# Optimization experiments

Hardware: AMD Instinct MI355X
Metric: run time of the kernel (lower is better)

The kernel has to match this reference:

```python
import jax, jax.numpy as jnp
import numpy as np

WS = 8          # window_size
WSU = 2 * WS    # window_size_up
HEADS = 8
SHIFT = WS // 2


def _build_idx(nH, nW):
    # Faithful reproduction of the torch window-reordering index (static numpy).
    if nH % 2 == 0:
        idx_H = np.arange(nH).reshape(2, -1).transpose(1, 0).reshape(-1)
    else:
        idx_H = np.arange(nH + 1).reshape(2, -1).transpose(1, 0).reshape(-1)[:-1]
    if nW % 2 == 0:
        idx_W = np.arange(nW).reshape(2, -1).transpose(1, 0).reshape(-1)
    else:
        idx_W = np.arange(nW + 1).reshape(2, -1).transpose(1, 0).reshape(-1)[:-1]
    idx = np.array([list(idx_W + i * nW) for i in range(nW)])
    return np.asarray(idx[list(idx_H)].reshape(-1))


def _rel_pos_index():
    # coords over the query window offset by ws//2; reference coords over the 2ws x 2ws KV window
    ch = np.arange(WS // 2, WS + WS // 2)
    cw = np.arange(WS // 2, WS + WS // 2)
    coords = np.stack(np.meshgrid(ch, cw, indexing='ij')).reshape(2, -1)        # (2, 64)
    rh = np.arange(2 * WS)
    rw = np.arange(2 * WS)
    ref = np.stack(np.meshgrid(rh, rw, indexing='ij')).reshape(2, -1)           # (2, 256)
    rel = coords[:, :, None] - ref[:, None, :]                                  # (2, 64, 256)
    rel = rel.transpose(1, 2, 0).copy()
    rel[..., 0] += 2 * WS - 1
    rel[..., 1] += 2 * WS - 1
    rel[..., 0] *= 4 * WS - 1
    return rel.sum(-1)  # (64, 256)


def setup_inputs() -> dict:
    key = jax.random.key(0)
    ks = jax.random.split(key, 4)
    C = 256
    return {
        'x': jax.random.normal(ks[0], (8, 128, 128, C), dtype=jnp.float32),
        'mask': jnp.zeros((1, 1, 1), dtype=jnp.float32),  # unused by the module's forward
        'qkv_w': jax.random.normal(ks[1], (3 * C, C), dtype=jnp.float32) * 0.02,
        'qkv_b': jnp.zeros((3 * C,), dtype=jnp.float32),
        'proj_w': jax.random.normal(ks[2], (C, C), dtype=jnp.float32) * 0.02,
        'proj_b': jnp.zeros((C,), dtype=jnp.float32),
        'rel_table': jax.random.normal(ks[3], ((4 * WS - 1) * (4 * WS - 1), HEADS), dtype=jnp.float32) * 0.02,
    }


def reference(x, mask, qkv_w, qkv_b, proj_w, proj_b, rel_table):
    B, H, W, C = x.shape
    hd = C // HEADS
    scale = hd ** (-0.5)

    pad_b = (WS - H % WS) % WS
    pad_r = (WS - W % WS) % WS
    x = jnp.pad(x, ((0, 0), (0, pad_b), (0, pad_r), (0, 0)))
    Hp, Wp = H + pad_b, W + pad_r

    qkv = (x @ qkv_w.T + qkv_b).reshape(B, Hp, Wp, 3, C)
    q = qkv[..., 0, :]                                    # (B, Hp, Wp, C)
    kv = jnp.moveaxis(qkv[..., 1:, :], 3, 0)              # (2, B, Hp, Wp, C)

    # pad KV for cross-window context
    kv = jnp.pad(kv, ((0, 0), (0, 0), (SHIFT, WS - SHIFT), (SHIFT, WS - SHIFT), (0, 0)))
    Hpkv, Wpkv = Hp + WS, Wp + WS

    nH, nW = Hp // WS, Wp // WS
    nHs, nWs = Hpkv // WSU, Wpkv // WSU
    nHsh, nWsh = nH - nHs, nW - nWs

    kv1 = kv[:, :, :nHs * WSU, :nWs * WSU]
    kv2 = kv[:, :, :nHs * WSU, WS:WS + nWsh * WSU]
    kv3 = kv[:, :, WS:WS + nHsh * WSU, :nWs * WSU]
    kv4 = kv[:, :, WS:WS + nHsh * WSU, WS:WS + nWsh * WSU]
    cross = jnp.concatenate([jnp.concatenate([kv1, kv2], axis=3),
                             jnp.concatenate([kv3, kv4], axis=3)], axis=2)

    # window partition at WSU -> (2, B, nH*nW, WSU*WSU, C), then reorder windows
    cross = cross.reshape(2, B, nH, WSU, nW, WSU, C).transpose(0, 1, 2, 4, 3, 5, 6)
    cross = cross.reshape(2, B, nH * nW, WSU * WSU, C)
    cross = cross[:, :, _build_idx(nH, nW)]

    Bw = B * nH * nW
    M = WSU * WSU  # 4*WS*WS KV tokens per window
    N = WS * WS    # query tokens per window
    k = cross[0].reshape(Bw, M, HEADS, hd)
    v = cross[1].reshape(Bw, M, HEADS, hd)

    qw = q.reshape(B, nH, WS, nW, WS, C).transpose(0, 1, 3, 2, 4, 5).reshape(Bw, N, HEADS, hd)

    attn = jnp.einsum('bnhd,bmhd->bhnm', qw * scale, k)   # (Bw, HEADS, N, M)
    bias = rel_table[_rel_pos_index()]                    # (N, M, HEADS)
    attn = jax.nn.softmax(attn + bias.transpose(2, 0, 1)[None], axis=-1)

    out = jnp.einsum('bhnm,bmhd->bnhd', attn, v).reshape(Bw, N, C)
    out = out @ proj_w.T + proj_b

    out = out.reshape(B, nH, nW, WS, WS, C).transpose(0, 1, 3, 2, 4, 5).reshape(B, Hp, Wp, C)
    return out[:, :H, :W, :].reshape(B, H * W, C)
```

## Files before the change

### kernel.cpp

```cpp
#include <hip/hip_runtime.h>
#include <hip/hip_bf16.h>
#include <stdint.h>

typedef __bf16 bf16;
typedef __bf16 bf16x4 __attribute__((ext_vector_type(4)));
typedef __bf16 bf16x8 __attribute__((ext_vector_type(8)));
typedef float f32x4 __attribute__((ext_vector_type(4)));

#define MFMA_BF16(a, b, c) __builtin_amdgcn_mfma_f32_16x16x32_bf16((a), (b), (c), 0, 0, 0)

#define LOG2E 1.4426950408889634f
#define QSCALE (0.17677669529663687f * 1.4426950408889634f)

__device__ __forceinline__ void load16f(const float* p, float* r) {
#pragma unroll
  for (int i = 0; i < 4; ++i) {
    float4 v = *(const float4*)(p + 4 * i);
    r[4 * i + 0] = v.x; r[4 * i + 1] = v.y; r[4 * i + 2] = v.z; r[4 * i + 3] = v.w;
  }
}

__device__ __forceinline__ void store16_bf16(bf16* dst, const float* r) {
  bf16x8 v0, v1;
#pragma unroll
  for (int i = 0; i < 8; ++i) { v0[i] = (bf16)r[i]; v1[i] = (bf16)r[8 + i]; }
  *(bf16x8*)(dst) = v0;
  *(bf16x8*)(dst + 8) = v1;
}

__global__ __launch_bounds__(256)
void cvt_bf16(const float* __restrict__ X, const float* __restrict__ Wq,
              bf16* __restrict__ Xb, bf16* __restrict__ Wqb)
{
  const unsigned t = blockIdx.x * 256 + threadIdx.x;
  const float* src;
  bf16* dst;
  if (t < 4194304u) { src = X + (size_t)t * 8; dst = Xb + (size_t)t * 8; }
  else {
    const unsigned u = t - 4194304u;
    src = Wq + (size_t)u * 8; dst = Wqb + (size_t)u * 8;
  }
  const float4 a = ((const float4*)src)[0];
  const float4 b = ((const float4*)src)[1];
  bf16x8 v;
  v[0] = (bf16)a.x; v[1] = (bf16)a.y; v[2] = (bf16)a.z; v[3] = (bf16)a.w;
  v[4] = (bf16)b.x; v[5] = (bf16)b.y; v[6] = (bf16)b.z; v[7] = (bf16)b.w;
  *(bf16x8*)dst = v;
}

__global__ void bias_pre(const float* __restrict__ rel, float* __restrict__ biasC)
{
  const int t = blockIdx.x * 256 + threadIdx.x;
  const int li = t & 15, g = (t >> 4) & 3, kt = (t >> 6) & 15;
  const int qt = (t >> 10) & 3, h = (t >> 12) & 7;
  const int n = qt * 16 + li, ni = n >> 3, nj = n & 7;
  float4 v;
  float* vp = (float*)&v;
#pragma unroll
  for (int r = 0; r < 4; ++r) {
    const int key = 32 * (kt >> 1) + 8 * g + 4 * (kt & 1) + r;
    const int ki = key >> 4, kj = key & 15;
    const int bi = (ni + 19 - ki) * 31 + (nj + 19 - kj);
    vp[r] = rel[bi * 8 + h] * LOG2E;
  }
  ((float4*)biasC)[t] = v;
}

__global__ __launch_bounds__(256, 2)
void qkv_gemm(const bf16* __restrict__ X, const bf16* __restrict__ W,
              const float* __restrict__ bias,
              bf16* __restrict__ Qb, bf16* __restrict__ Kb, bf16* __restrict__ Vg)
{
  constexpr int K = 256;
  constexpr int LD = 40;
  __shared__ bf16 As[128 * LD];
  __shared__ bf16 Bs[128 * LD];

  const int tid = threadIdx.x;
  const int lane = tid & 63, wave = tid >> 6;
  const int bn = blockIdx.x % 6, bm = blockIdx.x / 6;
  const int m0 = bm * 128, n0 = bn * 128;
  const int sr = tid >> 1, sc = (tid & 1) * 16;
  const int wr = (wave >> 1) * 64, wc = (wave & 1) * 64;
  const int g = lane >> 4, li = lane & 15;

  const f32x4 fzero = {0.f, 0.f, 0.f, 0.f};
  f32x4 acc[4][4];
#pragma unroll
  for (int i = 0; i < 4; ++i)
#pragma unroll
    for (int j = 0; j < 4; ++j) acc[i][j] = fzero;

  const bf16* Ap = X + (size_t)(m0 + sr) * K + sc;
  const bf16* Bp = W + (size_t)(n0 + sr) * K + sc;
  uint4 aV0, aV1, bV0, bV1;
  aV0 = *(const uint4*)(Ap); aV1 = *(const uint4*)(Ap + 8);
  bV0 = *(const uint4*)(Bp); bV1 = *(const uint4*)(Bp + 8);

#pragma unroll 1
  for (int kt = 0; kt < 8; ++kt) {
    *(uint4*)&As[sr * LD + sc] = aV0;
    *(uint4*)&As[sr * LD + sc + 8] = aV1;
    *(uint4*)&Bs[sr * LD + sc] = bV0;
    *(uint4*)&Bs[sr * LD + sc + 8] = bV1;
    __syncthreads();
    if (kt < 7) {
      Ap += 32; Bp += 32;
      aV0 = *(const uint4*)(Ap); aV1 = *(const uint4*)(Ap + 8);
      bV0 = *(const uint4*)(Bp); bV1 = *(const uint4*)(Bp + 8);
    }
    bf16x8 af[4], bfr[4];
#pragma unroll
    for (int t = 0; t < 4; ++t) {
      af[t]  = *(const bf16x8*)&As[(wr + t * 16 + li) * LD + g * 8];
      bfr[t] = *(const bf16x8*)&Bs[(wc + t * 16 + li) * LD + g * 8];
    }
#pragma unroll
    for (int i = 0; i < 4; ++i)
#pragma unroll
      for (int j = 0; j < 4; ++j)
        acc[i][j] = MFMA_BF16(af[i], bfr[j], acc[i][j]);
    __syncthreads();
  }

#pragma unroll
  for (int i = 0; i < 4; ++i) {
    const int row = m0 + wr + i * 16 + g * 4;
#pragma unroll
    for (int j = 0; j < 4; ++j) {
      const int col = n0 + wc + j * 16 + li;
      const float bv = bias[col];
      const int which = col >> 8;
      if (which == 2) {
        const int hh = (col >> 5) & 7, d = col & 31;
        bf16x4 pv;
#pragma unroll
        for (int r = 0; r < 4; ++r) pv[r] = (bf16)(acc[i][j][r] + bv);
        *(bf16x4*)(Vg + (((size_t)hh) << 22) + (size_t)(row >> 2) * 128 + d * 4) = pv;
      } else {
        bf16* dst = which == 0 ? Qb : Kb;
        const float sc2 = which == 0 ? QSCALE : 1.0f;
        const size_t base = (size_t)((col >> 5) & 7) * (131072u * 32u) + (size_t)(col & 31);
#pragma unroll
        for (int r = 0; r < 4; ++r)
          dst[base + (size_t)(row + r) * 32u] = (bf16)((acc[i][j][r] + bv) * sc2);
      }
    }
  }
}

__global__ __launch_bounds__(256, 4)
void win_attn(const bf16* __restrict__ Qb, const bf16* __restrict__ Kb,
              const bf16* __restrict__ Vg, const float* __restrict__ biasC,
              bf16* __restrict__ Ob)
{
  constexpr int LDK = 40;
  __shared__ bf16 Ks[256 * LDK];

  const int tid = threadIdx.x;
  const int lane = tid & 63, qt = tid >> 6;
  const int li = lane & 15, g = lane >> 4;
  const int bid = blockIdx.x;
  const int h = bid & 7, w = bid >> 3;
  const int b = w >> 8, wi = (w >> 4) & 15, wj = w & 15;
  const int btok = b << 14;

  const int q = qt * 16 + li;
  const int tokq = btok + (wi * 8 + (q >> 3)) * 128 + (wj * 8 + (q & 7));
  const bf16x8 qf = *(const bf16x8*)(Qb + ((((size_t)h) << 17) + tokq) * 32 + g * 8);

  {
    const size_t hb = ((size_t)h) << 17;
#pragma unroll
    for (int it = 0; it < 4; ++it) {
      const int u = it * 256 + tid;
      const int m = u >> 2, c = u & 3;
      const int hi = m >> 4, hj = m & 15;
      const int gi = wi * 8 - 4 + hi, gj = wj * 8 - 4 + hj;
      const bool ok = ((unsigned)gi < 128u) && ((unsigned)gj < 128u);
      uint4 kv{};
      if (ok) kv = *(const uint4*)(Kb + (hb + (size_t)(btok + gi * 128 + gj)) * 32 + c * 8);
      const int si = ((hi & 1) << 3) | ((hj >> 3) << 2) | (hj & 3);
      const int kt = ((hi >> 1) << 1) | ((hj >> 2) & 1);
      *(uint4*)&Ks[(kt * 16 + si) * LDK + c * 8] = kv;
    }
  }
  __syncthreads();

  const float* bC = biasC + (size_t)(((h * 4 + qt) * 16 * 4 + g) * 16 + li) * 4;
  f32x4 s[16];
#pragma unroll
  for (int kt = 0; kt < 16; ++kt) {
    const f32x4 c0 = *(const f32x4*)(bC + kt * 256);
    const bf16x8 kf = *(const bf16x8*)&Ks[(kt * 16 + li) * LDK + g * 8];
    s[kt] = MFMA_BF16(kf, qf, c0);
  }

  const f32x4 z4 = {0.f, 0.f, 0.f, 0.f};
  f32x4 o0 = z4, o1 = z4, o2 = z4;
  const bf16 one1 = (bf16)1.0f;
  const bf16x8 vones = {one1, one1, one1, one1, one1, one1, one1, one1};

  const int g1 = g & 1, g2 = g >> 1;
  const int gj0 = wj * 8 - 4 + 8 * g1;
  const bool c0ok = (unsigned)gj0 < 128u;
  const bool c1ok = (unsigned)(gj0 + 4) < 128u;
  const int gi0 = wi * 8 - 4 + g2;
  const bf16* vb = Vg + (((size_t)h) << 22) + (size_t)(btok >> 2) * 128 + li * 4;
  const int q4a = gj0 >> 2;

#pragma unroll
  for (int ks = 0; ks < 8; ++ks) {
    const int gi = gi0 + 2 * ks;
    const bool rok = (unsigned)gi < 128u;
    bf16x4 a0{}, a1{}, b0{}, b1{};
    if (rok & c0ok) {
      const bf16* p = vb + (size_t)(gi * 32 + q4a) * 128;
      a0 = *(const bf16x4*)p;
      b0 = *(const bf16x4*)(p + 64);
    }
    if (rok & c1ok) {
      const bf16* p = vb + (size_t)(gi * 32 + q4a + 1) * 128;
      a1 = *(const bf16x4*)p;
      b1 = *(const bf16x4*)(p + 64);
    }
    bf16x8 pb;
#pragma unroll
    for (int u = 0; u < 4; ++u) {
      pb[u]     = (bf16)exp2f(s[2 * ks][u]);
      pb[u + 4] = (bf16)exp2f(s[2 * ks + 1][u]);
    }
    const bf16x8 vf0 = __builtin_shufflevector(a0, a1, 0, 1, 2, 3, 4, 5, 6, 7);
    const bf16x8 vf1 = __builtin_shufflevector(b0, b1, 0, 1, 2, 3, 4, 5, 6, 7);
    o0 = MFMA_BF16(vf0, pb, o0);
    o1 = MFMA_BF16(vf1, pb, o1);
    o2 = MFMA_BF16(vones, pb, o2);
  }
  const float inv = __builtin_amdgcn_rcpf(o2[0]);

  bf16* op = Ob + (size_t)tokq * 256 + h * 32 + 4 * g;
  bf16x4 w0, w1;
#pragma unroll
  for (int r = 0; r < 4; ++r) {
    w0[r] = (bf16)(o0[r] * inv);
    w1[r] = (bf16)(o1[r] * inv);
  }
  *(bf16x4*)(op) = w0;
  *(bf16x4*)(op + 16) = w1;
}

__global__ __launch_bounds__(256, 2)
void proj_gemm(const bf16* __restrict__ A, const float* __restrict__ W,
               const float* __restrict__ bias, float* __restrict__ Out)
{
  constexpr int K = 256;
  constexpr int LD = 40;
  __shared__ bf16 As[128 * LD];
  __shared__ bf16 Bs[128 * LD];

  const int tid = threadIdx.x;
  const int lane = tid & 63, wave = tid >> 6;
  const int bn = blockIdx.x & 1, bm = blockIdx.x >> 1;
  const int m0 = bm * 128, n0 = bn * 128;
  const int sr = tid >> 1, sc = (tid & 1) * 16;
  const int wr = (wave >> 1) * 64, wc = (wave & 1) * 64;
  const int g = lane >> 4, li = lane & 15;

  const f32x4 fzero = {0.f, 0.f, 0.f, 0.f};
  f32x4 acc[4][4];
#pragma unroll
  for (int i = 0; i < 4; ++i)
#pragma unroll
    for (int j = 0; j < 4; ++j) acc[i][j] = fzero;

  const bf16* Ap = A + (size_t)(m0 + sr) * K + sc;
  const float* Bp = W + (size_t)(n0 + sr) * K + sc;
  uint4 aV0, aV1; float bR[16];
  aV0 = *(const uint4*)(Ap); aV1 = *(const uint4*)(Ap + 8);
  load16f(Bp, bR);

#pragma unroll 1
  for (int kt = 0; kt < 8; ++kt) {
    *(uint4*)&As[sr * LD + sc] = aV0;
    *(uint4*)&As[sr * LD + sc + 8] = aV1;
    store16_bf16(&Bs[sr * LD + sc], bR);
    __syncthreads();
    if (kt < 7) {
      Ap += 32; Bp += 32;
      aV0 = *(const uint4*)(Ap); aV1 = *(const uint4*)(Ap + 8);
      load16f(Bp, bR);
    }
    bf16x8 af[4], bfr[4];
#pragma unroll
    for (int t = 0; t < 4; ++t) {
      af[t]  = *(const bf16x8*)&As[(wr + t * 16 + li) * LD + g * 8];
      bfr[t] = *(const bf16x8*)&Bs[(wc + t * 16 + li) * LD + g * 8];
    }
#pragma unroll
    for (int i = 0; i < 4; ++i)
#pragma unroll
      for (int j = 0; j < 4; ++j)
        acc[i][j] = MFMA_BF16(af[i], bfr[j], acc[i][j]);
    __syncthreads();
  }

#pragma unroll
  for (int i = 0; i < 4; ++i) {
    const int row = m0 + wr + i * 16 + g * 4;
#pragma unroll
    for (int j = 0; j < 4; ++j) {
      const int col = n0 + wc + j * 16 + li;
      const float bv = bias[col];
#pragma unroll
      for (int r = 0; r < 4; ++r)
        Out[(size_t)(row + r) * 256 + col] = acc[i][j][r] + bv;
    }
  }
}

extern "C" void kernel_launch(void* const* d_in, const int* in_sizes, int n_in,
                              void* d_out, int out_size, void* d_ws, size_t ws_size,
                              hipStream_t stream)
{
  const float* x       = (const float*)d_in[0];
  const float* qkv_w   = (const float*)d_in[2];
  const float* qkv_b   = (const float*)d_in[3];
  const float* proj_w  = (const float*)d_in[4];
  const float* proj_b  = (const float*)d_in[5];
  const float* rel_tab = (const float*)d_in[6];
  float* out = (float*)d_out;

  char* ws = (char*)d_ws;
  bf16* Qb = (bf16*)(ws);
  bf16* Kb = (bf16*)(ws + (size_t)67108864);
  bf16* Vg = (bf16*)(ws + (size_t)134217728);
  bf16* Ao = (bf16*)(ws + (size_t)201326592);
  bf16* Xb = Ao;
  float* biasC = (float*)d_out;
  bf16*  Wqb   = (bf16*)((char*)d_out + 1048576);

  cvt_bf16<<<dim3(16480), dim3(256), 0, stream>>>(x, qkv_w, Xb, Wqb);
  bias_pre<<<dim3(128), dim3(256), 0, stream>>>(rel_tab, biasC);
  qkv_gemm<<<dim3(6144), dim3(256), 0, stream>>>(Xb, Wqb, qkv_b, Qb, Kb, Vg);
  win_attn<<<dim3(16384), dim3(256), 0, stream>>>(Qb, Kb, Vg, biasC, Ao);
  proj_gemm<<<dim3(2048), dim3(256), 0, stream>>>(Ao, proj_w, proj_b, out);
}
```

Before: 329.6 us.

## Store V in zero-padded halo layout so attention loads it without bounds checks

The QKV GEMM now writes V into a padded per-(head,batch) buffer with a 4-token zero border, stored inside the output buffer. A new vzero kernel clears the border regions. The attention kernel then issues unconditional 16-byte V loads before the barrier, overlapping them with the K staging, and drops the per-row and per-column bounds checks. In exchange it adds an extra kernel launch, holds more registers (occupancy hint lowered from 4 to 3), and uses the output buffer as scratch.

```diff
diff --git a/kernel.cpp b/kernel.cpp
--- a/kernel.cpp
+++ b/kernel.cpp
@@ -12,6 +12,9 @@
 #define LOG2E 1.4426950408889634f
 #define QSCALE (0.17677669529663687f * 1.4426950408889634f)
 
+#define VP_HB 591872
+#define VP_ROW 4352
+
 __device__ __forceinline__ void load16f(const float* p, float* r) {
 #pragma unroll
   for (int i = 0; i < 4; ++i) {
@@ -26,6 +29,29 @@
   for (int i = 0; i < 8; ++i) { v0[i] = (bf16)r[i]; v1[i] = (bf16)r[8 + i]; }
   *(bf16x8*)(dst) = v0;
   *(bf16x8*)(dst + 8) = v1;
+}
+
+__global__ __launch_bounds__(256)
+void vzero(bf16* __restrict__ Vp)
+{
+  const unsigned t = blockIdx.x * 256 + threadIdx.x;
+  size_t addr;
+  if (t < 557056u) {
+    const unsigned c2 = t & 1, d = (t >> 1) & 31;
+    const unsigned x = t >> 6;
+    const unsigned blk = x % 17u, rw = x / 17u;
+    const unsigned hb = rw >> 3, r8 = rw & 7;
+    const unsigned row = r8 < 4 ? r8 : r8 + 128;
+    addr = (size_t)hb * VP_HB + (size_t)row * VP_ROW + blk * 256 + d * 8 + c2 * 4;
+  } else {
+    const unsigned u = t - 557056u;
+    const unsigned d = u & 31, row4 = (u >> 5) & 127;
+    const unsigned pos = (u >> 12) & 1, hb = u >> 13;
+    addr = (size_t)hb * VP_HB + (size_t)(row4 + 4) * VP_ROW
+         + (pos ? 16 * 256 : 0) + d * 8 + (pos ? 4 : 0);
+  }
+  uint2 z{0u, 0u};
+  *(uint2*)(Vp + addr) = z;
 }
 
 __global__ __launch_bounds__(256)
@@ -69,7 +95,7 @@
 __global__ __launch_bounds__(256, 2)
 void qkv_gemm(const bf16* __restrict__ X, const bf16* __restrict__ W,
               const float* __restrict__ bias,
-              bf16* __restrict__ Qb, bf16* __restrict__ Kb, bf16* __restrict__ Vg)
+              bf16* __restrict__ Qb, bf16* __restrict__ Kb, bf16* __restrict__ Vp)
 {
   constexpr int K = 256;
   constexpr int LD = 40;
@@ -136,7 +162,11 @@
         bf16x4 pv;
 #pragma unroll
         for (int r = 0; r < 4; ++r) pv[r] = (bf16)(acc[i][j][r] + bv);
-        *(bf16x4*)(Vg + (((size_t)hh) << 22) + (size_t)(row >> 2) * 128 + d * 4) = pv;
+        const int bb = row >> 14, gi = (row >> 7) & 127, gj = row & 127;
+        const int cs = gj + 4;
+        bf16* dst = Vp + (size_t)(hh * 8 + bb) * VP_HB + (size_t)(gi + 4) * VP_ROW
+                  + (cs >> 3) * 256 + d * 8 + (cs & 7);
+        *(bf16x4*)dst = pv;
       } else {
         bf16* dst = which == 0 ? Qb : Kb;
         const float sc2 = which == 0 ? QSCALE : 1.0f;
@@ -149,9 +179,9 @@
   }
 }
 
-__global__ __launch_bounds__(256, 4)
+__global__ __launch_bounds__(256, 3)
 void win_attn(const bf16* __restrict__ Qb, const bf16* __restrict__ Kb,
-              const bf16* __restrict__ Vg, const float* __restrict__ biasC,
+              const bf16* __restrict__ Vp, const float* __restrict__ biasC,
               bf16* __restrict__ Ob)
 {
   constexpr int LDK = 40;
@@ -185,6 +215,18 @@
       *(uint4*)&Ks[(kt * 16 + si) * LDK + c * 8] = kv;
     }
   }
+
+  const int g1 = g & 1, g2 = g >> 1;
+  const bf16* vp = Vp + (size_t)(h * 8 + b) * VP_HB
+                 + (size_t)(wi * 8 + g2) * VP_ROW
+                 + (wj + g1) * 256 + li * 8;
+  bf16x8 va0[8], va1[8];
+#pragma unroll
+  for (int ks = 0; ks < 8; ++ks) {
+    va0[ks] = *(const bf16x8*)(vp + ks * (2 * VP_ROW));
+    va1[ks] = *(const bf16x8*)(vp + ks * (2 * VP_ROW) + 128);
+  }
+
   __syncthreads();
 
   const float* bC = biasC + (size_t)(((h * 4 + qt) * 16 * 4 + g) * 16 + li) * 4;
@@ -200,40 +242,16 @@
   f32x4 o0 = z4, o1 = z4, o2 = z4;
   const bf16 one1 = (bf16)1.0f;
   const bf16x8 vones = {one1, one1, one1, one1, one1, one1, one1, one1};
-
-  const int g1 = g & 1, g2 = g >> 1;
-  const int gj0 = wj * 8 - 4 + 8 * g1;
-  const bool c0ok = (unsigned)gj0 < 128u;
-  const bool c1ok = (unsigned)(gj0 + 4) < 128u;
-  const int gi0 = wi * 8 - 4 + g2;
-  const bf16* vb = Vg + (((size_t)h) << 22) + (size_t)(btok >> 2) * 128 + li * 4;
-  const int q4a = gj0 >> 2;
-
 #pragma unroll
   for (int ks = 0; ks < 8; ++ks) {
-    const int gi = gi0 + 2 * ks;
-    const bool rok = (unsigned)gi < 128u;
-    bf16x4 a0{}, a1{}, b0{}, b1{};
-    if (rok & c0ok) {
-      const bf16* p = vb + (size_t)(gi * 32 + q4a) * 128;
-      a0 = *(const bf16x4*)p;
-      b0 = *(const bf16x4*)(p + 64);
-    }
-    if (rok & c1ok) {
-      const bf16* p = vb + (size_t)(gi * 32 + q4a + 1) * 128;
-      a1 = *(const bf16x4*)p;
-      b1 = *(const bf16x4*)(p + 64);
-    }
     bf16x8 pb;
 #pragma unroll
     for (int u = 0; u < 4; ++u) {
       pb[u]     = (bf16)exp2f(s[2 * ks][u]);
       pb[u + 4] = (bf16)exp2f(s[2 * ks + 1][u]);
     }
-    const bf16x8 vf0 = __builtin_shufflevector(a0, a1, 0, 1, 2, 3, 4, 5, 6, 7);
-    const bf16x8 vf1 = __builtin_shufflevector(b0, b1, 0, 1, 2, 3, 4, 5, 6, 7);
-    o0 = MFMA_BF16(vf0, pb, o0);
-    o1 = MFMA_BF16(vf1, pb, o1);
+    o0 = MFMA_BF16(va0[ks], pb, o0);
+    o1 = MFMA_BF16(va1[ks], pb, o1);
     o2 = MFMA_BF16(vones, pb, o2);
   }
   const float inv = __builtin_amdgcn_rcpf(o2[0]);
@@ -333,15 +351,16 @@
   char* ws = (char*)d_ws;
   bf16* Qb = (bf16*)(ws);
   bf16* Kb = (bf16*)(ws + (size_t)67108864);
-  bf16* Vg = (bf16*)(ws + (size_t)134217728);
+  bf16* Xb = (bf16*)(ws + (size_t)134217728);
   bf16* Ao = (bf16*)(ws + (size_t)201326592);
-  bf16* Xb = Ao;
   float* biasC = (float*)d_out;
   bf16*  Wqb   = (bf16*)((char*)d_out + 1048576);
-
+  bf16*  Vp    = (bf16*)((char*)d_out + 2097152);
+
+  vzero<<<dim3(4224), dim3(256), 0, stream>>>(Vp);
   cvt_bf16<<<dim3(16480), dim3(256), 0, stream>>>(x, qkv_w, Xb, Wqb);
   bias_pre<<<dim3(128), dim3(256), 0, stream>>>(rel_tab, biasC);
-  qkv_gemm<<<dim3(6144), dim3(256), 0, stream>>>(Xb, Wqb, qkv_b, Qb, Kb, Vg);
-  win_attn<<<dim3(16384), dim3(256), 0, stream>>>(Qb, Kb, Vg, biasC, Ao);
+  qkv_gemm<<<dim3(6144), dim3(256), 0, stream>>>(Xb, Wqb, qkv_b, Qb, Kb, Vp);
+  win_attn<<<dim3(16384), dim3(256), 0, stream>>>(Qb, Kb, Vp, biasC, Ao);
   proj_gemm<<<dim3(2048), dim3(256), 0, stream>>>(Ao, proj_w, proj_b, out);
 }
```

New measurement: 358.5 us. 8.7% more time.
